# Kernel tuning notes

Measured on AMD Instinct MI355X. Metric: run time of the kernel, lower is better.

The kernel has to match this reference:

```python
import jax, jax.numpy as jnp
import numpy as np

B, P, F, D = 1024, 128, 512, 256
THETA = 1e-7  # numerical-stability constant (ratio-model denominator)


def setup_inputs() -> dict:
    key = jax.random.key(0)
    k1, k2, k3 = jax.random.split(key, 3)
    # xavier_uniform limits for [P, D] and [F, D] parameter matrices
    lim_p = float(np.sqrt(6.0 / (P + D)))
    lim_f = float(np.sqrt(6.0 / (F + D)))
    return {
        "x": jax.random.normal(k1, (B, D), dtype=jnp.float32),
        "prototypes": jax.random.uniform(k2, (P, D), jnp.float32, -lim_p, lim_p),
        "feature_bank": jax.random.uniform(k3, (F, D), jnp.float32, -lim_f, lim_f),
        "alpha": jnp.float32(0.5),
        "beta": jnp.float32(0.5),
    }


def reference(x, prototypes, feature_bank, alpha, beta):
    # Feature memberships: an object 'has' feature w iff <obj, w> > 0.
    xf = x @ feature_bank.T            # [B, F]
    pf = prototypes @ feature_bank.T   # [P, F]
    # Intersection, 'product' reduction: sum_k x_k * p_k over features both have.
    # x_k * 1[x_k>0] = relu(x_k), so this is a single GEMM of the relu'd memberships.
    inter = jnp.einsum("bf,pf->bp", jax.nn.relu(xf), jax.nn.relu(pf))  # [B, P]
    # Differences, 'substractmatch' reduction: over features both objects have,
    # sum of how much more membership one side has than the other.
    both = (xf > 0)[:, None, :] & (pf > 0)[None, :, :]   # [B, P, F]
    diff = xf[:, None, :] - pf[None, :, :]               # [B, P, F]
    zero = jnp.zeros((), dtype=xf.dtype)
    x_minus_p = jnp.sum(jnp.where(both & (diff > 0), diff, zero), axis=-1)   # [B, P]
    p_minus_x = jnp.sum(jnp.where(both & (diff < 0), -diff, zero), axis=-1)  # [B, P]
    # Tversky ratio-model similarity with theta for numerical stability.
    return inter / (inter + alpha * x_minus_p + beta * p_minus_x + THETA)
```

## Files before the change

### kernel.cpp

```cpp
#include <hip/hip_runtime.h>

#define Bn 1024
#define Pn 128
#define Fn 512
#define Dn 256
#define THETA 1e-7f
#define F16_MINN 6.103515625e-5f

typedef _Float16 f16;
typedef f16 f16x8 __attribute__((ext_vector_type(8)));
typedef f16 f16x4 __attribute__((ext_vector_type(4)));
typedef f16 f16x2 __attribute__((ext_vector_type(2)));
typedef float f32x4 __attribute__((ext_vector_type(4)));

#if defined(__has_builtin)
#if __has_builtin(__builtin_amdgcn_fdot2)
#define FDOT2(a, b, c) __builtin_amdgcn_fdot2((a), (b), (c), false)
#endif
#endif
#ifndef FDOT2
#define FDOT2(a, b, c) ((float)(a)[0] * (float)(b)[0] + (float)(a)[1] * (float)(b)[1] + (c))
#endif

__device__ __forceinline__ f16x2 get2(const f16x8 v, int idx) {
    union { f16x8 v8; f16x2 v2[4]; } u;
    u.v8 = v;
    return u.v2[idx];
}

__global__ __launch_bounds__(256)
void gemm_feat(const float* __restrict__ x, const float* __restrict__ prot,
               const float* __restrict__ fb,
               f16* __restrict__ RX, f16* __restrict__ RPT8)
{
    __shared__ float As[64][68];
    __shared__ float Fs[64][68];
    const int tid = threadIdx.x;
    const int rb  = blockIdx.y * 64;
    const int cb  = blockIdx.x * 64;
    const int tx  = tid & 15;
    const int ty  = tid >> 4;
    const int lr  = tid >> 2;
    const int lk  = tid & 3;

    float acc[4][4] = {};

    for (int k0 = 0; k0 < Dn; k0 += 64) {
        #pragma unroll
        for (int q = 0; q < 4; ++q) {
            const int kk = lk + q * 4;
            const int r  = rb + lr;
            const float* asrc = (r < Bn) ? (x + (size_t)r * Dn)
                                         : (prot + (size_t)(r - Bn) * Dn);
            float4 av = *(const float4*)(asrc + k0 + kk * 4);
            float4 fv = *(const float4*)(fb + (size_t)(cb + lr) * Dn + k0 + kk * 4);
            As[kk*4+0][lr] = av.x; As[kk*4+1][lr] = av.y;
            As[kk*4+2][lr] = av.z; As[kk*4+3][lr] = av.w;
            Fs[kk*4+0][lr] = fv.x; Fs[kk*4+1][lr] = fv.y;
            Fs[kk*4+2][lr] = fv.z; Fs[kk*4+3][lr] = fv.w;
        }
        __syncthreads();
        #pragma unroll 8
        for (int k = 0; k < 64; ++k) {
            float4 a = *(const float4*)&As[k][ty * 4];
            float4 f = *(const float4*)&Fs[k][tx * 4];
            const float aa[4] = {a.x, a.y, a.z, a.w};
            const float ff[4] = {f.x, f.y, f.z, f.w};
            #pragma unroll
            for (int i = 0; i < 4; ++i)
                #pragma unroll
                for (int j = 0; j < 4; ++j)
                    acc[i][j] = fmaf(aa[i], ff[j], acc[i][j]);
        }
        __syncthreads();
    }

    const f16 MINN = (f16)F16_MINN;
    #pragma unroll
    for (int i = 0; i < 4; ++i) {
        const int r = rb + ty * 4 + i;
        if (r < Bn) {
            f16x4 rv;
            #pragma unroll
            for (int j = 0; j < 4; ++j) {
                const float v = acc[i][j];
                f16 t = (f16)0;
                if (v > 0.f) { t = (f16)v; if (t < MINN) t = MINN; }
                rv[j] = t;
            }
            *(f16x4*)(RX + (size_t)r * Fn + cb + tx * 4) = rv;
        } else {
            const int p = r - Bn;
            #pragma unroll
            for (int j = 0; j < 4; ++j) {
                const int c = cb + tx * 4 + j;
                const float v = acc[i][j];
                f16 t = (f16)0;
                if (v > 0.f) { t = (f16)v; if (t < MINN) t = MINN; }
                RPT8[(size_t)(c >> 3) * (Pn * 8) + p * 8 + (c & 7)] = t;
            }
        }
    }
}

__global__ __launch_bounds__(256)
void tversky_main(const f16* __restrict__ RX, const f16* __restrict__ RPT8,
                  const float* __restrict__ alpha_p, const float* __restrict__ beta_p,
                  float* __restrict__ out)
{
    __shared__ f32x4 sAcc[16][256];
    const int tid   = threadIdx.x;
    const int ot    = tid & 15;
    const int slice = tid >> 4;
    const int bt    = ot >> 2;
    const int pt    = ot & 3;
    const int bb    = blockIdx.x * 16;
    const int pb    = blockIdx.y * 16;
    const int b0    = bb + bt * 4;
    const int p0    = pb + pt * 4;
    const int g0    = slice * 4;

    float aI[4][4] = {};
    float aM[4][4] = {};
    float aX[4][4] = {};
    float aP[4][4] = {};

    const f16x2 one2 = {(f16)1, (f16)1};
    f16x8 KS, ONE8;
    #pragma unroll
    for (int e = 0; e < 8; ++e) { KS[e] = (f16)65504.0f; ONE8[e] = (f16)1; }

    #pragma unroll
    for (int g = 0; g < 4; ++g) {
        const size_t xoff = (size_t)(g0 + g) * 8;
        f16x8 rx[4], bx[4];
        #pragma unroll
        for (int i = 0; i < 4; ++i) {
            rx[i] = *(const f16x8*)(RX + (size_t)(b0 + i) * Fn + xoff);
            bx[i] = __builtin_elementwise_min(rx[i] * KS, ONE8);
        }
        const size_t pbase = (size_t)(g0 + g) * (Pn * 8) + (size_t)p0 * 8;
        f16x8 rp[4], bp[4];
        #pragma unroll
        for (int q = 0; q < 4; ++q) {
            rp[q] = *(const f16x8*)(RPT8 + pbase + q * 8);
            bp[q] = __builtin_elementwise_min(rp[q] * KS, ONE8);
        }
        #pragma unroll
        for (int i = 0; i < 4; ++i) {
            #pragma unroll
            for (int q = 0; q < 4; ++q) {
                const f16x8 mn = __builtin_elementwise_min(rx[i], rp[q]);
                #pragma unroll
                for (int h = 0; h < 4; ++h) {
                    aI[i][q] = FDOT2(get2(rx[i], h), get2(rp[q], h), aI[i][q]);
                    aM[i][q] = FDOT2(get2(mn, h),    one2,           aM[i][q]);
                    aX[i][q] = FDOT2(get2(rx[i], h), get2(bp[q], h), aX[i][q]);
                    aP[i][q] = FDOT2(get2(bx[i], h), get2(rp[q], h), aP[i][q]);
                }
            }
        }
    }

    #pragma unroll
    for (int i = 0; i < 4; ++i) {
        #pragma unroll
        for (int q = 0; q < 4; ++q) {
            const int outIdx = (bt * 4 + i) * 16 + pt * 4 + q;
            f32x4 v = {aI[i][q], aM[i][q], aX[i][q], aP[i][q]};
            sAcc[slice][outIdx] = v;
        }
    }
    __syncthreads();

    {
        f32x4 acc = sAcc[0][tid];
        #pragma unroll
        for (int s = 1; s < 16; ++s) acc += sAcc[s][tid];
        const float alpha = *alpha_p;
        const float beta  = *beta_p;
        const float I = acc[0], M = acc[1], X = acc[2], P = acc[3];
        const float W = alpha * (X - M) + beta * (P - M);
        const int brow = tid >> 4, pcol = tid & 15;
        out[(size_t)(bb + brow) * Pn + pb + pcol] = I / (I + W + THETA);
    }
}

extern "C" void kernel_launch(void* const* d_in, const int* in_sizes, int n_in,
                              void* d_out, int out_size, void* d_ws, size_t ws_size,
                              hipStream_t stream)
{
    const float* x     = (const float*)d_in[0];
    const float* prot  = (const float*)d_in[1];
    const float* fb    = (const float*)d_in[2];
    const float* alpha = (const float*)d_in[3];
    const float* beta  = (const float*)d_in[4];
    float* out = (float*)d_out;

    f16* RX   = (f16*)d_ws;
    f16* RPT8 = RX + (size_t)Bn * Fn;

    dim3 gg(Fn / 64, (Bn + Pn) / 64);
    gemm_feat<<<gg, 256, 0, stream>>>(x, prot, fb, RX, RPT8);

    dim3 gm(Bn / 16, Pn / 16);
    tversky_main<<<gm, 256, 0, stream>>>(RX, RPT8, alpha, beta, out);
}
```

Baseline: 27.66 us.

## Use packed f16 accumulation in Tversky main loop with per-epoch float flush

Replaces the fdot2 f32-accumulating inner loop with packed f16x2 fma/min accumulators, which are flushed into float sums after every two feature groups. The thread tiling changes from 4x4 outputs over 16 slices to 2x4 outputs over 8 slices, so each thread covers more features and the shared-memory reduction shrinks. Packed f16 math can issue two lanes per instruction and halves the cross-slice reduction work. In exchange, partial sums of up to 16 products are kept in f16, which loses precision and could overflow.

```diff
diff --git a/kernel.cpp b/kernel.cpp
--- a/kernel.cpp
+++ b/kernel.cpp
@@ -12,21 +12,6 @@
 typedef f16 f16x4 __attribute__((ext_vector_type(4)));
 typedef f16 f16x2 __attribute__((ext_vector_type(2)));
 typedef float f32x4 __attribute__((ext_vector_type(4)));
-
-#if defined(__has_builtin)
-#if __has_builtin(__builtin_amdgcn_fdot2)
-#define FDOT2(a, b, c) __builtin_amdgcn_fdot2((a), (b), (c), false)
-#endif
-#endif
-#ifndef FDOT2
-#define FDOT2(a, b, c) ((float)(a)[0] * (float)(b)[0] + (float)(a)[1] * (float)(b)[1] + (c))
-#endif
-
-__device__ __forceinline__ f16x2 get2(const f16x8 v, int idx) {
-    union { f16x8 v8; f16x2 v2[4]; } u;
-    u.v8 = v;
-    return u.v2[idx];
-}
 
 __global__ __launch_bounds__(256)
 void gemm_feat(const float* __restrict__ x, const float* __restrict__ prot,
@@ -108,75 +93,85 @@
                   const float* __restrict__ alpha_p, const float* __restrict__ beta_p,
                   float* __restrict__ out)
 {
-    __shared__ f32x4 sAcc[16][256];
+    __shared__ f32x4 sAcc[8][256];
     const int tid   = threadIdx.x;
-    const int ot    = tid & 15;
-    const int slice = tid >> 4;
+    const int ot    = tid & 31;
+    const int slice = tid >> 5;
     const int bt    = ot >> 2;
     const int pt    = ot & 3;
     const int bb    = blockIdx.x * 16;
     const int pb    = blockIdx.y * 16;
-    const int b0    = bb + bt * 4;
+    const int b0    = bb + bt * 2;
     const int p0    = pb + pt * 4;
-    const int g0    = slice * 4;
-
-    float aI[4][4] = {};
-    float aM[4][4] = {};
-    float aX[4][4] = {};
-    float aP[4][4] = {};
-
-    const f16x2 one2 = {(f16)1, (f16)1};
+    const int g0    = slice * 8;
+
+    float fI[2][4] = {}, fM[2][4] = {}, fX[2][4] = {}, fP[2][4] = {};
+
     f16x8 KS, ONE8;
     #pragma unroll
     for (int e = 0; e < 8; ++e) { KS[e] = (f16)65504.0f; ONE8[e] = (f16)1; }
 
     #pragma unroll
-    for (int g = 0; g < 4; ++g) {
-        const size_t xoff = (size_t)(g0 + g) * 8;
-        f16x8 rx[4], bx[4];
-        #pragma unroll
-        for (int i = 0; i < 4; ++i) {
-            rx[i] = *(const f16x8*)(RX + (size_t)(b0 + i) * Fn + xoff);
-            bx[i] = __builtin_elementwise_min(rx[i] * KS, ONE8);
-        }
-        const size_t pbase = (size_t)(g0 + g) * (Pn * 8) + (size_t)p0 * 8;
-        f16x8 rp[4], bp[4];
+    for (int ep = 0; ep < 4; ++ep) {
+        f16x2 aI[2][4] = {}, aM[2][4] = {}, aX[2][4] = {}, aP[2][4] = {};
+        #pragma unroll
+        for (int gg = 0; gg < 2; ++gg) {
+            const int g = g0 + ep * 2 + gg;
+            f16x2 rx2[2][4], bx2[2][4], rp2[4][4], bp2[4][4];
+            #pragma unroll
+            for (int i = 0; i < 2; ++i) {
+                const f16x8 v = *(const f16x8*)(RX + (size_t)(b0 + i) * Fn + (size_t)g * 8);
+                const f16x8 m = __builtin_elementwise_min(v * KS, ONE8);
+                const f16x4 vl = v.lo, vh = v.hi, ml = m.lo, mh = m.hi;
+                rx2[i][0] = vl.lo; rx2[i][1] = vl.hi; rx2[i][2] = vh.lo; rx2[i][3] = vh.hi;
+                bx2[i][0] = ml.lo; bx2[i][1] = ml.hi; bx2[i][2] = mh.lo; bx2[i][3] = mh.hi;
+            }
+            const size_t pbase = (size_t)g * (Pn * 8) + (size_t)p0 * 8;
+            #pragma unroll
+            for (int q = 0; q < 4; ++q) {
+                const f16x8 v = *(const f16x8*)(RPT8 + pbase + q * 8);
+                const f16x8 m = __builtin_elementwise_min(v * KS, ONE8);
+                const f16x4 vl = v.lo, vh = v.hi, ml = m.lo, mh = m.hi;
+                rp2[q][0] = vl.lo; rp2[q][1] = vl.hi; rp2[q][2] = vh.lo; rp2[q][3] = vh.hi;
+                bp2[q][0] = ml.lo; bp2[q][1] = ml.hi; bp2[q][2] = mh.lo; bp2[q][3] = mh.hi;
+            }
+            #pragma unroll
+            for (int i = 0; i < 2; ++i)
+                #pragma unroll
+                for (int q = 0; q < 4; ++q)
+                    #pragma unroll
+                    for (int h = 0; h < 4; ++h) {
+                        aI[i][q] = __builtin_elementwise_fma(rx2[i][h], rp2[q][h], aI[i][q]);
+                        aM[i][q] = aM[i][q] + __builtin_elementwise_min(rx2[i][h], rp2[q][h]);
+                        aX[i][q] = __builtin_elementwise_fma(rx2[i][h], bp2[q][h], aX[i][q]);
+                        aP[i][q] = __builtin_elementwise_fma(bx2[i][h], rp2[q][h], aP[i][q]);
+                    }
+        }
+        #pragma unroll
+        for (int i = 0; i < 2; ++i)
+            #pragma unroll
+            for (int q = 0; q < 4; ++q) {
+                fI[i][q] += (float)aI[i][q][0] + (float)aI[i][q][1];
+                fM[i][q] += (float)aM[i][q][0] + (float)aM[i][q][1];
+                fX[i][q] += (float)aX[i][q][0] + (float)aX[i][q][1];
+                fP[i][q] += (float)aP[i][q][0] + (float)aP[i][q][1];
+            }
+    }
+
+    #pragma unroll
+    for (int i = 0; i < 2; ++i)
         #pragma unroll
         for (int q = 0; q < 4; ++q) {
-            rp[q] = *(const f16x8*)(RPT8 + pbase + q * 8);
-            bp[q] = __builtin_elementwise_min(rp[q] * KS, ONE8);
-        }
-        #pragma unroll
-        for (int i = 0; i < 4; ++i) {
-            #pragma unroll
-            for (int q = 0; q < 4; ++q) {
-                const f16x8 mn = __builtin_elementwise_min(rx[i], rp[q]);
-                #pragma unroll
-                for (int h = 0; h < 4; ++h) {
-                    aI[i][q] = FDOT2(get2(rx[i], h), get2(rp[q], h), aI[i][q]);
-                    aM[i][q] = FDOT2(get2(mn, h),    one2,           aM[i][q]);
-                    aX[i][q] = FDOT2(get2(rx[i], h), get2(bp[q], h), aX[i][q]);
-                    aP[i][q] = FDOT2(get2(bx[i], h), get2(rp[q], h), aP[i][q]);
-                }
-            }
-        }
-    }
-
-    #pragma unroll
-    for (int i = 0; i < 4; ++i) {
-        #pragma unroll
-        for (int q = 0; q < 4; ++q) {
-            const int outIdx = (bt * 4 + i) * 16 + pt * 4 + q;
-            f32x4 v = {aI[i][q], aM[i][q], aX[i][q], aP[i][q]};
+            const int outIdx = (bt * 2 + i) * 16 + pt * 4 + q;
+            f32x4 v = {fI[i][q], fM[i][q], fX[i][q], fP[i][q]};
             sAcc[slice][outIdx] = v;
         }
-    }
     __syncthreads();
 
     {
         f32x4 acc = sAcc[0][tid];
         #pragma unroll
-        for (int s = 1; s < 16; ++s) acc += sAcc[s][tid];
+        for (int s = 1; s < 8; ++s) acc += sAcc[s][tid];
         const float alpha = *alpha_p;
         const float beta  = *beta_p;
         const float I = acc[0], M = acc[1], X = acc[2], P = acc[3];
```

New measurement: 29.79 us. 7.7% more time.
